# Performance work log

Hardware: AMD Instinct MI355X
Metric: run time of the kernel (lower is better)

Reference implementation:

```python
import jax, jax.numpy as jnp
import numpy as np

N_BINS = 15
N = 1_000_000
C = 100


def setup_inputs() -> dict:
    key = jax.random.key(0)
    k1, k2 = jax.random.split(key)
    logits = jax.random.normal(k1, (N, C), dtype=jnp.float32)
    labels = jax.random.randint(k2, (N,), 0, C, dtype=jnp.int64)
    return {"logits": logits, "labels": labels}


def reference(logits, labels):
    # sigmoid then per-row max/argmax (NOT softmax; faithful to original)
    sigmoids = jax.nn.sigmoid(logits)
    confidences = jnp.max(sigmoids, axis=1)            # [N]
    predictions = jnp.argmax(sigmoids, axis=1)         # [N]
    accuracies = (predictions == labels).astype(jnp.float32)

    # bin i covers (boundaries[i], boundaries[i+1]] ; searchsorted 'left'
    # finds first boundary >= conf, so bin = idx - 1.
    boundaries = jnp.linspace(0.0, 1.0, N_BINS + 1)
    bin_idx = jnp.clip(
        jnp.searchsorted(boundaries, confidences, side="left") - 1, 0, N_BINS - 1
    )

    n = confidences.shape[0]
    ones = jnp.ones_like(confidences)
    counts = jax.ops.segment_sum(ones, bin_idx, num_segments=N_BINS)        # samples per bin
    conf_sum = jax.ops.segment_sum(confidences, bin_idx, num_segments=N_BINS)
    acc_sum = jax.ops.segment_sum(accuracies, bin_idx, num_segments=N_BINS)

    safe_counts = jnp.maximum(counts, 1.0)
    avg_conf = conf_sum / safe_counts
    avg_acc = acc_sum / safe_counts
    prop = counts / jnp.float32(n)
    # original accumulates signed (avg_conf - avg_acc) * prop, skipping empty bins
    per_bin = jnp.where(counts > 0, (avg_conf - avg_acc) * prop, 0.0)
    ece = jnp.sum(per_bin)
    return ece
```

## Files before the change

### kernel.cpp

```cpp
#include <hip/hip_runtime.h>
#include <math.h>


#define N_ROWS 1000000
#define N_COLS 100
#define BLOCK 256
#define ROWS_PER_BLOCK (BLOCK / 4)
#define N_BLOCKS (N_ROWS / ROWS_PER_BLOCK)

__global__ __launch_bounds__(BLOCK) void ece_main(
    const float* __restrict__ logits,
    const int* __restrict__ labels,
    double* __restrict__ partials)
{
    const int t   = threadIdx.x;
    const int gid = blockIdx.x * BLOCK + t;
    const int row = gid >> 2;
    const int q   = gid & 3;

    const float4* rowp = reinterpret_cast<const float4*>(logits + (size_t)row * N_COLS);

    float vmax = -INFINITY;
    int   imax = 0;
#pragma unroll
    for (int k = 0; k < 6; ++k) {
        const int i4 = q + 4 * k;
        const float4 v = rowp[i4];
        const int c = i4 * 4;
        if (v.x > vmax) { vmax = v.x; imax = c;     }
        if (v.y > vmax) { vmax = v.y; imax = c + 1; }
        if (v.z > vmax) { vmax = v.z; imax = c + 2; }
        if (v.w > vmax) { vmax = v.w; imax = c + 3; }
    }
    if (q == 0) {
        const float4 v = rowp[24];
        if (v.x > vmax) { vmax = v.x; imax = 96; }
        if (v.y > vmax) { vmax = v.y; imax = 97; }
        if (v.z > vmax) { vmax = v.z; imax = 98; }
        if (v.w > vmax) { vmax = v.w; imax = 99; }
    }

#pragma unroll
    for (int m = 1; m <= 2; m <<= 1) {
        const float vo = __shfl_xor(vmax, m, 4);
        const int   io = __shfl_xor(imax, m, 4);
        if (vo > vmax || (vo == vmax && io < imax)) { vmax = vo; imax = io; }
    }

    double s = 0.0;
    if (q == 0) {
        const float conf = 1.0f / (1.0f + expf(-vmax));
        const float acc  = (imax == labels[row]) ? 1.0f : 0.0f;
        s = (double)conf - (double)acc;
    }

#pragma unroll
    for (int off = 32; off > 0; off >>= 1) s += __shfl_down(s, off, 64);

    __shared__ double wsum[BLOCK / 64];
    if ((t & 63) == 0) wsum[t >> 6] = s;
    __syncthreads();
    if (t == 0) {
        double b = 0.0;
#pragma unroll
        for (int w = 0; w < BLOCK / 64; ++w) b += wsum[w];
        partials[blockIdx.x] = b;
    }
}

__global__ __launch_bounds__(BLOCK) void ece_finalize(
    const double* __restrict__ partials, int nb, float* __restrict__ out)
{
    double s = 0.0;
    for (int i = threadIdx.x; i < nb; i += BLOCK) s += partials[i];
#pragma unroll
    for (int off = 32; off > 0; off >>= 1) s += __shfl_down(s, off, 64);

    __shared__ double wsum[BLOCK / 64];
    if ((threadIdx.x & 63) == 0) wsum[threadIdx.x >> 6] = s;
    __syncthreads();
    if (threadIdx.x == 0) {
        double b = 0.0;
#pragma unroll
        for (int w = 0; w < BLOCK / 64; ++w) b += wsum[w];
        out[0] = (float)(b / (double)N_ROWS);
    }
}

extern "C" void kernel_launch(void* const* d_in, const int* in_sizes, int n_in,
                              void* d_out, int out_size, void* d_ws, size_t ws_size,
                              hipStream_t stream)
{
    const float* logits = (const float*)d_in[0];
    const int*   labels = (const int*)d_in[1];
    float*       out    = (float*)d_out;
    double*      partials = (double*)d_ws;

    ece_main<<<N_BLOCKS, BLOCK, 0, stream>>>(logits, labels, partials);
    ece_finalize<<<1, BLOCK, 0, stream>>>(partials, N_BLOCKS, out);
}
```

Measured before the change: 523.9 us.

## Use 16 lanes per row with grid-stride tiles and nontemporal loads

Each row is now read by 16 lanes instead of 4, so a row's 400 bytes arrive as mostly contiguous float4 loads rather than strided ones. The kernel becomes a fixed 2500-block grid-stride loop, which cuts the number of per-block partial sums. Logit reads use nontemporal loads to avoid polluting the cache. Partials are accumulated in float rather than double, which is slightly less precise. Lanes 9 to 15 sit idle during the second load, and only one lane in 16 does the sigmoid and label check.

Result: slower. 535.8 us (+2.3%).

```diff
diff --git a/kernel.cpp b/kernel.cpp
--- a/kernel.cpp
+++ b/kernel.cpp
@@ -5,63 +5,65 @@
 #define N_ROWS 1000000
 #define N_COLS 100
 #define BLOCK 256
-#define ROWS_PER_BLOCK (BLOCK / 4)
-#define N_BLOCKS (N_ROWS / ROWS_PER_BLOCK)
+#define ROWS_PER_TILE (BLOCK / 16)
+#define N_TILES (N_ROWS / ROWS_PER_TILE)
+#define GRID 2500
+
+typedef float vfloat4 __attribute__((ext_vector_type(4)));
 
 __global__ __launch_bounds__(BLOCK) void ece_main(
     const float* __restrict__ logits,
     const int* __restrict__ labels,
-    double* __restrict__ partials)
+    float* __restrict__ partials)
 {
-    const int t   = threadIdx.x;
-    const int gid = blockIdx.x * BLOCK + t;
-    const int row = gid >> 2;
-    const int q   = gid & 3;
+    const int t = threadIdx.x;
+    const int r = t >> 4;
+    const int l = t & 15;
 
-    const float4* rowp = reinterpret_cast<const float4*>(logits + (size_t)row * N_COLS);
+    float local = 0.0f;
 
-    float vmax = -INFINITY;
-    int   imax = 0;
+    for (int tile = blockIdx.x; tile < N_TILES; tile += GRID) {
+        const int row = tile * ROWS_PER_TILE + r;
+        const vfloat4* rowp = reinterpret_cast<const vfloat4*>(
+            logits + (size_t)row * N_COLS);
+
+        const vfloat4 a = __builtin_nontemporal_load(rowp + l);
+        float vmax = a.x; int imax = 4 * l;
+        if (a.y > vmax) { vmax = a.y; imax = 4 * l + 1; }
+        if (a.z > vmax) { vmax = a.z; imax = 4 * l + 2; }
+        if (a.w > vmax) { vmax = a.w; imax = 4 * l + 3; }
+
+        if (l < 9) {
+            const vfloat4 b = __builtin_nontemporal_load(rowp + 16 + l);
+            const int c = 64 + 4 * l;
+            if (b.x > vmax) { vmax = b.x; imax = c;     }
+            if (b.y > vmax) { vmax = b.y; imax = c + 1; }
+            if (b.z > vmax) { vmax = b.z; imax = c + 2; }
+            if (b.w > vmax) { vmax = b.w; imax = c + 3; }
+        }
+
 #pragma unroll
-    for (int k = 0; k < 6; ++k) {
-        const int i4 = q + 4 * k;
-        const float4 v = rowp[i4];
-        const int c = i4 * 4;
-        if (v.x > vmax) { vmax = v.x; imax = c;     }
-        if (v.y > vmax) { vmax = v.y; imax = c + 1; }
-        if (v.z > vmax) { vmax = v.z; imax = c + 2; }
-        if (v.w > vmax) { vmax = v.w; imax = c + 3; }
-    }
-    if (q == 0) {
-        const float4 v = rowp[24];
-        if (v.x > vmax) { vmax = v.x; imax = 96; }
-        if (v.y > vmax) { vmax = v.y; imax = 97; }
-        if (v.z > vmax) { vmax = v.z; imax = 98; }
-        if (v.w > vmax) { vmax = v.w; imax = 99; }
+        for (int m = 1; m <= 8; m <<= 1) {
+            const float vo = __shfl_xor(vmax, m, 16);
+            const int   io = __shfl_xor(imax, m, 16);
+            if (vo > vmax || (vo == vmax && io < imax)) { vmax = vo; imax = io; }
+        }
+
+        if (l == 0) {
+            const float conf = 1.0f / (1.0f + expf(-vmax));
+            const float acc  = (imax == labels[row]) ? 1.0f : 0.0f;
+            local += conf - acc;
+        }
     }
 
 #pragma unroll
-    for (int m = 1; m <= 2; m <<= 1) {
-        const float vo = __shfl_xor(vmax, m, 4);
-        const int   io = __shfl_xor(imax, m, 4);
-        if (vo > vmax || (vo == vmax && io < imax)) { vmax = vo; imax = io; }
-    }
+    for (int off = 32; off > 0; off >>= 1) local += __shfl_down(local, off, 64);
 
-    double s = 0.0;
-    if (q == 0) {
-        const float conf = 1.0f / (1.0f + expf(-vmax));
-        const float acc  = (imax == labels[row]) ? 1.0f : 0.0f;
-        s = (double)conf - (double)acc;
-    }
-
-#pragma unroll
-    for (int off = 32; off > 0; off >>= 1) s += __shfl_down(s, off, 64);
-
-    __shared__ double wsum[BLOCK / 64];
-    if ((t & 63) == 0) wsum[t >> 6] = s;
+    __shared__ float wsum[BLOCK / 64];
+    if ((t & 63) == 0) wsum[t >> 6] = local;
     __syncthreads();
     if (t == 0) {
-        double b = 0.0;
+        float b = 0.0f;
 #pragma unroll
         for (int w = 0; w < BLOCK / 64; ++w) b += wsum[w];
         partials[blockIdx.x] = b;
@@ -69,10 +71,10 @@
 }
 
 __global__ __launch_bounds__(BLOCK) void ece_finalize(
-    const double* __restrict__ partials, int nb, float* __restrict__ out)
+    const float* __restrict__ partials, float* __restrict__ out)
 {
     double s = 0.0;
-    for (int i = threadIdx.x; i < nb; i += BLOCK) s += partials[i];
+    for (int i = threadIdx.x; i < GRID; i += BLOCK) s += (double)partials[i];
 #pragma unroll
     for (int off = 32; off > 0; off >>= 1) s += __shfl_down(s, off, 64);
 
@@ -94,8 +96,8 @@
     const float* logits = (const float*)d_in[0];
     const int*   labels = (const int*)d_in[1];
     float*       out    = (float*)d_out;
-    double*      partials = (double*)d_ws;
+    float*       partials = (float*)d_ws;
 
-    ece_main<<<N_BLOCKS, BLOCK, 0, stream>>>(logits, labels, partials);
-    ece_finalize<<<1, BLOCK, 0, stream>>>(partials, N_BLOCKS, out);
+    ece_main<<<GRID, BLOCK, 0, stream>>>(logits, labels, partials);
+    ece_finalize<<<1, BLOCK, 0, stream>>>(partials, out);
 }
```
